# Optimization experiments

Measured on AMD Instinct MI355X. Metric: run time of the kernel, lower is better.

Reference implementation:

```python
import jax, jax.numpy as jnp
import numpy as np

NUM_EMBEDDINGS = 4096
EMBEDDING_DIM = 64
COMMITMENT_COST = 0.25
DECAY = 0.99
EPSILON = 1e-05


def setup_inputs() -> dict:
    key = jax.random.key(0)
    k1, k2, k3, k4 = jax.random.split(key, 4)
    z = jax.random.normal(k1, (128, 24, 1536), dtype=jnp.float32)
    embedding = jax.random.normal(k2, (NUM_EMBEDDINGS, EMBEDDING_DIM), dtype=jnp.float32) * 0.05
    ema_cluster_size = jax.random.uniform(k3, (NUM_EMBEDDINGS,), dtype=jnp.float32)
    ema_w = jax.random.normal(k4, (NUM_EMBEDDINGS, EMBEDDING_DIM), dtype=jnp.float32) * 0.05
    return {"z": z, "embedding": embedding, "ema_cluster_size": ema_cluster_size, "ema_w": ema_w}


def reference(z, embedding, ema_cluster_size, ema_w):
    # VectorQuantizer.forward in training mode (EMA codebook update).
    K, d = embedding.shape
    B = z.shape[0]
    z_flat = z.reshape(-1, d)  # [N, d], N = B*576

    # Pairwise squared distances: ||z||^2 + ||e||^2 - 2 z e^T  -> [N, K]
    dist = (jnp.sum(z_flat * z_flat, axis=1, keepdims=True)
            + jnp.sum(embedding * embedding, axis=1)
            - 2.0 * (z_flat @ embedding.T))
    codes = jnp.argmin(dist, axis=1)  # [N]

    # EMA statistics (one-hot scatter expressed as segment sums)
    counts = jax.ops.segment_sum(jnp.ones_like(codes, dtype=z.dtype), codes, num_segments=K)
    new_cluster_size = DECAY * ema_cluster_size + (1.0 - DECAY) * counts
    dw = jax.ops.segment_sum(z_flat, codes, num_segments=K)  # [K, d]
    new_ema_w = DECAY * ema_w + (1.0 - DECAY) * dw

    n = jnp.sum(new_cluster_size)
    cluster_size = (new_cluster_size + EPSILON) / (n + K * EPSILON) * n
    new_embedding = new_ema_w / cluster_size[:, None]

    # Quantize with the UPDATED codebook (torch copies weights before embedding lookup)
    z_q = new_embedding[codes].reshape(z.shape)
    vq_loss = COMMITMENT_COST * jnp.mean((jax.lax.stop_gradient(z_q) - z) ** 2)
    z_q_st = z + jax.lax.stop_gradient(z_q - z)  # straight-through
    codes = codes.reshape(B, -1)  # [B, 576]
    return (vq_loss, z_q_st, codes, new_embedding, new_cluster_size, new_ema_w)
```

## Files before the change

### kernel.cpp

```cpp
#include <hip/hip_runtime.h>

constexpr int KC    = 4096;
constexpr int DIM   = 64;
constexpr int NROWS = 73728;
constexpr int NELEM = 4718592;
constexpr int GSTRIDE = 4160;

typedef _Float16 f16x8 __attribute__((ext_vector_type(8)));
typedef float    f32x4 __attribute__((ext_vector_type(4)));

constexpr size_t OUT_LOSS  = 0;
constexpr size_t OUT_ZQ    = 1;
constexpr size_t OUT_CODES = 1 + (size_t)NELEM;
constexpr size_t OUT_EMB   = OUT_CODES + (size_t)NROWS;
constexpr size_t OUT_NCS   = OUT_EMB + (size_t)KC * DIM;
constexpr size_t OUT_NEW   = OUT_NCS + (size_t)KC;

constexpr size_t alignup(size_t x, size_t a) { return (x + a - 1) & ~(a - 1); }
constexpr size_t WS_CODES  = 0;
constexpr size_t WS_COUNTS = WS_CODES + sizeof(int) * (size_t)NROWS;
constexpr size_t WS_OFFS   = WS_COUNTS + sizeof(int) * (size_t)KC;
constexpr size_t WS_CURSOR = alignup(WS_OFFS + sizeof(int) * (KC + 1), 16);
constexpr size_t WS_SORTED = WS_CURSOR + sizeof(int) * (size_t)KC;
constexpr size_t WS_N      = alignup(WS_SORTED + sizeof(int) * (size_t)NROWS, 16);
constexpr size_t WS_LOSSD  = alignup(WS_N + sizeof(float), 8);
constexpr size_t WS_EMBPK  = alignup(WS_LOSSD + 8, 64);

__global__ void k_prep(const float* __restrict__ emb, char* __restrict__ emb_pk,
                       int* __restrict__ counts) {
    if (threadIdx.x < 32) counts[blockIdx.x * 32 + threadIdx.x] = 0;
    int t = blockIdx.x * 256 + threadIdx.x;
    int c = t >> 3, q = t & 7;
    const float* ep = emb + (size_t)c * DIM + q * 8;
    f16x8 hv, lv;
    float s = 0.f;
    #pragma unroll
    for (int e = 0; e < 8; ++e) {
        float x = ep[e];
        _Float16 h = (_Float16)x;
        float r = x - (float)h;
        hv[e] = h;
        lv[e] = (_Float16)(r * 2048.0f);
        s = fmaf(x, x, s);
    }
    s += __shfl_xor(s, 1, 64);
    s += __shfl_xor(s, 2, 64);
    s += __shfl_xor(s, 4, 64);
    int g = c >> 4, lc = c & 15;
    int h = q >> 2, lq = q & 3;
    int lane = lq * 16 + lc;
    char* gbase = emb_pk + (size_t)g * GSTRIDE;
    if (q == 0) *(float*)(gbase + lc * 4) = 1024.0f * s;
    char* base = gbase + 64 + lane * 16;
    *(f16x8*)(base + h * 1024)       = hv;
    *(f16x8*)(base + (2 + h) * 1024) = lv;
}

__global__ __launch_bounds__(192, 2) void k_argmin7(
        const float* __restrict__ z, const char* __restrict__ emb_pk,
        int* __restrict__ codes_i, float* __restrict__ codes_f,
        int* __restrict__ counts) {
    __shared__ int codebuf[3][48];

    const int tid = threadIdx.x;
    const int l   = tid & 63;
    const int w   = tid >> 6;
    const int lc  = l & 15;
    const int lq  = l >> 4;
    const int waveRow = blockIdx.x * 144 + w * 48;

    f16x8 ah2k[3][2], ahr[3][2], al2k[3][2];
    #pragma unroll
    for (int rt = 0; rt < 3; ++rt)
        #pragma unroll
        for (int h = 0; h < 2; ++h) {
            const float* zp = z + (size_t)(waveRow + rt * 16 + lc) * DIM + h * 32 + lq * 8;
            float4 x0 = *(const float4*)zp;
            float4 x1 = *(const float4*)(zp + 4);
            float xs[8] = {x0.x, x0.y, x0.z, x0.w, x1.x, x1.y, x1.z, x1.w};
            #pragma unroll
            for (int e = 0; e < 8; ++e) {
                _Float16 hh = (_Float16)xs[e];
                float rr = xs[e] - (float)hh;
                ahr[rt][h][e]  = -hh;
                ah2k[rt][h][e] = (_Float16)(-2048.0f * (float)hh);
                al2k[rt][h][e] = -(_Float16)(rr * 2048.0f);
            }
        }

    float best[3][4];
    int   bestg[3][4];
    #pragma unroll
    for (int rt = 0; rt < 3; ++rt)
        #pragma unroll
        for (int j = 0; j < 4; ++j) { best[rt][j] = INFINITY; bestg[rt][j] = 0; }

    const unsigned long long pkb = (unsigned long long)emb_pk;
    unsigned voffA = 64 + l * 16;
    unsigned voffB = lc * 4;

    f16x8 b00, b01, b02, b03, b10, b11, b12, b13;
    f16x8 b20, b21, b22, b23, b30, b31, b32, b33;
    float e0, e1, e2v, e3;

#define ISSUE(B0, B1, B2, B3, EV)                                                        \
    asm volatile("global_load_dword %0, %1, %2"             : "=v"(EV) : "v"(voffB), "s"(pkb)); \
    asm volatile("global_load_dwordx4 %0, %1, %2"             : "=v"(B0) : "v"(voffA), "s"(pkb)); \
    asm volatile("global_load_dwordx4 %0, %1, %2 offset:1024" : "=v"(B1) : "v"(voffA), "s"(pkb)); \
    asm volatile("global_load_dwordx4 %0, %1, %2 offset:2048" : "=v"(B2) : "v"(voffA), "s"(pkb)); \
    asm volatile("global_load_dwordx4 %0, %1, %2 offset:3072" : "=v"(B3) : "v"(voffA), "s"(pkb)); \
    voffA += GSTRIDE; voffB += GSTRIDE;

#define WAITP                                                \
    asm volatile("s_waitcnt vmcnt(15)" ::: "memory");        \
    __builtin_amdgcn_sched_barrier(0);

#define COMP(B0, B1, B2, B3, EV, G) {                                             \
        f32x4 ci; ci[0] = EV; ci[1] = EV; ci[2] = EV; ci[3] = EV;                 \
        _Pragma("unroll")                                                         \
        for (int rt = 0; rt < 3; ++rt) {                                          \
            f32x4 acc = __builtin_amdgcn_mfma_f32_16x16x32_f16(ah2k[rt][0], B0, ci, 0, 0, 0); \
            acc = __builtin_amdgcn_mfma_f32_16x16x32_f16(ah2k[rt][1], B1, acc, 0, 0, 0);      \
            acc = __builtin_amdgcn_mfma_f32_16x16x32_f16(ahr[rt][0],  B2, acc, 0, 0, 0);      \
            acc = __builtin_amdgcn_mfma_f32_16x16x32_f16(ahr[rt][1],  B3, acc, 0, 0, 0);      \
            acc = __builtin_amdgcn_mfma_f32_16x16x32_f16(al2k[rt][0], B0, acc, 0, 0, 0);      \
            acc = __builtin_amdgcn_mfma_f32_16x16x32_f16(al2k[rt][1], B1, acc, 0, 0, 0);      \
            _Pragma("unroll")                                                     \
            for (int j = 0; j < 4; ++j) {                                         \
                if (acc[j] < best[rt][j]) { best[rt][j] = acc[j]; bestg[rt][j] = (G); } \
            }                                                                     \
        } }

    __builtin_amdgcn_sched_barrier(0);
    ISSUE(b00, b01, b02, b03, e0)
    ISSUE(b10, b11, b12, b13, e1)
    ISSUE(b20, b21, b22, b23, e2v)
    ISSUE(b30, b31, b32, b33, e3)

    for (int g = 0; g < 256; g += 4) {
        WAITP  COMP(b00, b01, b02, b03, e0,  g)      ISSUE(b00, b01, b02, b03, e0)
        WAITP  COMP(b10, b11, b12, b13, e1,  g + 1)  ISSUE(b10, b11, b12, b13, e1)
        WAITP  COMP(b20, b21, b22, b23, e2v, g + 2)  ISSUE(b20, b21, b22, b23, e2v)
        WAITP  COMP(b30, b31, b32, b33, e3,  g + 3)  ISSUE(b30, b31, b32, b33, e3)
    }
    asm volatile("s_waitcnt vmcnt(0)" ::: "memory");
    __builtin_amdgcn_sched_barrier(0);
#undef ISSUE
#undef WAITP
#undef COMP

    #pragma unroll
    for (int rt = 0; rt < 3; ++rt)
        #pragma unroll
        for (int j = 0; j < 4; ++j) {
            float b = best[rt][j];
            int   k = bestg[rt][j] * 16 + lc;
            #pragma unroll
            for (int m = 1; m < 16; m <<= 1) {
                float obv = __shfl_xor(b, m, 64);
                int   okv = __shfl_xor(k, m, 64);
                if (obv < b || (obv == b && okv < k)) { b = obv; k = okv; }
            }
            if (lc == 0) codebuf[w][rt * 16 + lq * 4 + j] = k;
        }

    if (l < 48) {
        int code = codebuf[w][l];
        size_t rowg = (size_t)waveRow + l;
        codes_i[rowg] = code;
        codes_f[rowg] = (float)code;
        atomicAdd(&counts[code], 1);
    }
}

__global__ void k_scan(const int* __restrict__ counts,
                       int* __restrict__ offsets, int* __restrict__ cursor,
                       const float* __restrict__ ema_cs, float* __restrict__ ncs_out,
                       float* __restrict__ n_out, double* __restrict__ lossp) {
    __shared__ int   part[256];
    __shared__ float fpart[256];
    int tid = threadIdx.x;
    if (tid == 0) *lossp = 0.0;
    int base = tid * 16;
    int loc[16];
    int s = 0;
    float fs = 0.f;
    #pragma unroll
    for (int j = 0; j < 16; ++j) {
        int cnt = counts[base + j];
        loc[j] = s; s += cnt;
        float v = 0.99f * ema_cs[base + j] + 0.01f * (float)cnt;
        ncs_out[base + j] = v;
        fs += v;
    }
    part[tid] = s;
    fpart[tid] = fs;
    __syncthreads();
    for (int off = 1; off < 256; off <<= 1) {
        int v = (tid >= off) ? part[tid - off] : 0;
        __syncthreads();
        part[tid] += v;
        __syncthreads();
    }
    int excl = part[tid] - s;
    #pragma unroll
    for (int j = 0; j < 16; ++j) {
        int o = excl + loc[j];
        offsets[base + j] = o;
        cursor[base + j]  = o;
    }
    if (tid == 255) offsets[KC] = excl + s;
    for (int m = 128; m > 0; m >>= 1) {
        if (tid < m) fpart[tid] += fpart[tid + m];
        __syncthreads();
    }
    if (tid == 0) n_out[0] = fpart[0];
}

__global__ void k_scatteridx(const int* __restrict__ codes_i,
                             int* __restrict__ cursor, int* __restrict__ sorted_rows) {
    int r = blockIdx.x * 256 + threadIdx.x;
    if (r < NROWS) {
        int c = codes_i[r];
        int p = atomicAdd(&cursor[c], 1);
        sorted_rows[p] = r;
    }
}

__global__ __launch_bounds__(64) void k_dwsum(
        const float* __restrict__ z, const int* __restrict__ offsets,
        const int* __restrict__ sorted_rows, const float* __restrict__ ema_w,
        const float* __restrict__ ncs, const float* __restrict__ nptr,
        float* __restrict__ new_ema_w_out, float* __restrict__ new_emb_out) {
    int k = blockIdx.x, tid = threadIdx.x;
    int beg = offsets[k], end = offsets[k + 1];
    float a0 = 0.f, a1 = 0.f, a2 = 0.f, a3 = 0.f;
    int i = beg;
    for (; i + 3 < end; i += 4) {
        int r0 = sorted_rows[i], r1 = sorted_rows[i + 1];
        int r2 = sorted_rows[i + 2], r3 = sorted_rows[i + 3];
        a0 += z[(size_t)r0 * DIM + tid];
        a1 += z[(size_t)r1 * DIM + tid];
        a2 += z[(size_t)r2 * DIM + tid];
        a3 += z[(size_t)r3 * DIM + tid];
    }
    for (; i < end; ++i) a0 += z[(size_t)sorted_rows[i] * DIM + tid];
    float dwv = (a0 + a1) + (a2 + a3);
    size_t idx = (size_t)k * DIM + tid;
    float n = nptr[0];
    float nw = 0.99f * ema_w[idx] + 0.01f * dwv;
    float cs = (ncs[k] + 1e-5f) / (n + 4096.0f * 1e-5f) * n;
    new_ema_w_out[idx] = nw;
    new_emb_out[idx] = nw / cs;
}

__global__ __launch_bounds__(256) void k_quant(
        const float* __restrict__ z, const float* __restrict__ new_emb,
        const int* __restrict__ codes, float* __restrict__ zq_out,
        double* __restrict__ loss_acc) {
    __shared__ double red[256];
    const int nvec = NELEM / 4;
    int t = blockIdx.x * 256 + threadIdx.x;
    int stride = gridDim.x * 256;
    double ls = 0.0;
    for (int v = t; v < nvec; v += stride) {
        int e0 = v * 4;
        int n  = e0 >> 6;
        int d0 = e0 & 63;
        int code = codes[n];
        float4 zq = *(const float4*)&new_emb[(size_t)code * DIM + d0];
        float4 zv = *(const float4*)&z[e0];
        float dx = zq.x - zv.x, dy = zq.y - zv.y, dz = zq.z - zv.z, dw4 = zq.w - zv.w;
        float4 o;
        o.x = zv.x + dx; o.y = zv.y + dy; o.z = zv.z + dz; o.w = zv.w + dw4;
        *(float4*)&zq_out[e0] = o;
        ls += (double)(dx * dx) + (double)(dy * dy) + (double)(dz * dz) + (double)(dw4 * dw4);
    }
    red[threadIdx.x] = ls;
    __syncthreads();
    for (int m = 128; m > 0; m >>= 1) {
        if (threadIdx.x < m) red[threadIdx.x] += red[threadIdx.x + m];
        __syncthreads();
    }
    if (threadIdx.x == 0) atomicAdd(loss_acc, red[0]);
}

__global__ void k_loss(const double* __restrict__ loss_acc, float* __restrict__ out0) {
    out0[0] = (float)(0.25 * (loss_acc[0] / (double)NELEM));
}

extern "C" void kernel_launch(void* const* d_in, const int* in_sizes, int n_in,
                              void* d_out, int out_size, void* d_ws, size_t ws_size,
                              hipStream_t stream) {
    const float* z      = (const float*)d_in[0];
    const float* emb    = (const float*)d_in[1];
    const float* ema_cs = (const float*)d_in[2];
    const float* ema_w  = (const float*)d_in[3];
    float* out = (float*)d_out;
    char*  ws  = (char*)d_ws;

    int*    codes_i = (int*)(ws + WS_CODES);
    int*    counts  = (int*)(ws + WS_COUNTS);
    int*    offsets = (int*)(ws + WS_OFFS);
    int*    cursor  = (int*)(ws + WS_CURSOR);
    int*    sorted  = (int*)(ws + WS_SORTED);
    float*  nptr    = (float*)(ws + WS_N);
    double* lossp   = (double*)(ws + WS_LOSSD);
    char*   emb_pk  = ws + WS_EMBPK;

    k_prep<<<(KC * 8) / 256, 256, 0, stream>>>(emb, emb_pk, counts);
    k_argmin7<<<NROWS / 144, 192, 0, stream>>>(z, emb_pk, codes_i,
                                               out + OUT_CODES, counts);
    k_scan<<<1, 256, 0, stream>>>(counts, offsets, cursor, ema_cs,
                                  out + OUT_NCS, nptr, lossp);
    k_scatteridx<<<(NROWS + 255) / 256, 256, 0, stream>>>(codes_i, cursor, sorted);
    k_dwsum<<<KC, 64, 0, stream>>>(z, offsets, sorted, ema_w,
                                   out + OUT_NCS, nptr, out + OUT_NEW, out + OUT_EMB);
    k_quant<<<1152, 256, 0, stream>>>(z, out + OUT_EMB, codes_i,
                                      out + OUT_ZQ, lossp);
    k_loss<<<1, 1, 0, stream>>>(lossp, out + OUT_LOSS);
}
```

Measured before the change: 167.6 us.

## Stage codebook tiles into an LDS ring via direct global-to-LDS loads

The argmin kernel stops having every wave load the packed f16 codebook straight into registers. The three waves of a block now share a 12-slot LDS ring filled with global_load_lds DMA, and each wave reads operands back from LDS. The codebook norms move into a separate array that is preloaded whole into LDS. This removes the redundant per-wave global traffic for the codebook but adds a block barrier every four groups, LDS read latency, and roughly 64KB of LDS per block, which may limit occupancy to two blocks per CU.

```diff
diff --git a/kernel.cpp b/kernel.cpp
--- a/kernel.cpp
+++ b/kernel.cpp
@@ -4,7 +4,8 @@
 constexpr int DIM   = 64;
 constexpr int NROWS = 73728;
 constexpr int NELEM = 4718592;
-constexpr int GSTRIDE = 4160;
+constexpr int RB    = 4096;
+constexpr int RING  = 12;
 
 typedef _Float16 f16x8 __attribute__((ext_vector_type(8)));
 typedef float    f32x4 __attribute__((ext_vector_type(4)));
@@ -22,12 +23,19 @@
 constexpr size_t WS_OFFS   = WS_COUNTS + sizeof(int) * (size_t)KC;
 constexpr size_t WS_CURSOR = alignup(WS_OFFS + sizeof(int) * (KC + 1), 16);
 constexpr size_t WS_SORTED = WS_CURSOR + sizeof(int) * (size_t)KC;
-constexpr size_t WS_N      = alignup(WS_SORTED + sizeof(int) * (size_t)NROWS, 16);
+constexpr size_t WS_E2     = alignup(WS_SORTED + sizeof(int) * (size_t)NROWS, 64);
+constexpr size_t WS_N      = WS_E2 + sizeof(float) * (size_t)KC;
 constexpr size_t WS_LOSSD  = alignup(WS_N + sizeof(float), 8);
 constexpr size_t WS_EMBPK  = alignup(WS_LOSSD + 8, 64);
 
+__device__ __forceinline__ void gload16(const void* g, void* l) {
+    __builtin_amdgcn_global_load_lds(
+        (const __attribute__((address_space(1))) unsigned int*)g,
+        (__attribute__((address_space(3))) unsigned int*)l, 16, 0, 0);
+}
+
 __global__ void k_prep(const float* __restrict__ emb, char* __restrict__ emb_pk,
-                       int* __restrict__ counts) {
+                       float* __restrict__ e2s, int* __restrict__ counts) {
     if (threadIdx.x < 32) counts[blockIdx.x * 32 + threadIdx.x] = 0;
     int t = blockIdx.x * 256 + threadIdx.x;
     int c = t >> 3, q = t & 7;
@@ -46,21 +54,23 @@
     s += __shfl_xor(s, 1, 64);
     s += __shfl_xor(s, 2, 64);
     s += __shfl_xor(s, 4, 64);
+    if (q == 0) e2s[c] = 1024.0f * s;
     int g = c >> 4, lc = c & 15;
     int h = q >> 2, lq = q & 3;
     int lane = lq * 16 + lc;
-    char* gbase = emb_pk + (size_t)g * GSTRIDE;
-    if (q == 0) *(float*)(gbase + lc * 4) = 1024.0f * s;
-    char* base = gbase + 64 + lane * 16;
+    char* base = emb_pk + (size_t)g * RB + lane * 16;
     *(f16x8*)(base + h * 1024)       = hv;
     *(f16x8*)(base + (2 + h) * 1024) = lv;
 }
 
-__global__ __launch_bounds__(192, 2) void k_argmin7(
+__global__ __launch_bounds__(192, 2) void k_argmin8(
         const float* __restrict__ z, const char* __restrict__ emb_pk,
+        const float* __restrict__ e2s,
         int* __restrict__ codes_i, float* __restrict__ codes_f,
         int* __restrict__ counts) {
+    __shared__ __align__(16) char lds[RING * RB + 16384];
     __shared__ int codebuf[3][48];
+    constexpr int E2OFF = RING * RB;
 
     const int tid = threadIdx.x;
     const int l   = tid & 63;
@@ -95,25 +105,21 @@
         #pragma unroll
         for (int j = 0; j < 4; ++j) { best[rt][j] = INFINITY; bestg[rt][j] = 0; }
 
-    const unsigned long long pkb = (unsigned long long)emb_pk;
-    unsigned voffA = 64 + l * 16;
-    unsigned voffB = lc * 4;
-
-    f16x8 b00, b01, b02, b03, b10, b11, b12, b13;
-    f16x8 b20, b21, b22, b23, b30, b31, b32, b33;
-    float e0, e1, e2v, e3;
-
-#define ISSUE(B0, B1, B2, B3, EV)                                                        \
-    asm volatile("global_load_dword %0, %1, %2"             : "=v"(EV) : "v"(voffB), "s"(pkb)); \
-    asm volatile("global_load_dwordx4 %0, %1, %2"             : "=v"(B0) : "v"(voffA), "s"(pkb)); \
-    asm volatile("global_load_dwordx4 %0, %1, %2 offset:1024" : "=v"(B1) : "v"(voffA), "s"(pkb)); \
-    asm volatile("global_load_dwordx4 %0, %1, %2 offset:2048" : "=v"(B2) : "v"(voffA), "s"(pkb)); \
-    asm volatile("global_load_dwordx4 %0, %1, %2 offset:3072" : "=v"(B3) : "v"(voffA), "s"(pkb)); \
-    voffA += GSTRIDE; voffB += GSTRIDE;
-
-#define WAITP                                                \
-    asm volatile("s_waitcnt vmcnt(15)" ::: "memory");        \
-    __builtin_amdgcn_sched_barrier(0);
+#define STAGE(GS) {                                                         \
+        int slot_ = (GS) % RING;                                            \
+        int gsrc_ = (GS) < 256 ? (GS) : 255;                                \
+        const char* gp_ = emb_pk + (size_t)gsrc_ * RB + (l << 4);           \
+        char* lp_ = lds + slot_ * RB;                                       \
+        gload16(gp_ + w * 1024, lp_ + w * 1024);                            \
+        gload16(gp_ + 3072,     lp_ + 3072); }
+
+#define LOADL(EV, B0, B1, B2, B3, G) {                                      \
+        const char* p_ = lds + ((G) % RING) * RB + (l << 4);                \
+        B0 = *(const f16x8*)(p_);                                           \
+        B1 = *(const f16x8*)(p_ + 1024);                                    \
+        B2 = *(const f16x8*)(p_ + 2048);                                    \
+        B3 = *(const f16x8*)(p_ + 3072);                                    \
+        EV = *(const float*)(lds + E2OFF + (((G) * 16 + lc) << 2)); }
 
 #define COMP(B0, B1, B2, B3, EV, G) {                                             \
         f32x4 ci; ci[0] = EV; ci[1] = EV; ci[2] = EV; ci[3] = EV;                 \
@@ -131,22 +137,35 @@
             }                                                                     \
         } }
 
+    for (int s = w; s < 16; s += 3)
+        gload16((const char*)e2s + s * 1024 + (l << 4), lds + E2OFF + s * 1024);
+    for (int gs = 0; gs < 8; ++gs) STAGE(gs);
+    asm volatile("s_waitcnt vmcnt(16)" ::: "memory");
+    __builtin_amdgcn_s_barrier();
     __builtin_amdgcn_sched_barrier(0);
-    ISSUE(b00, b01, b02, b03, e0)
-    ISSUE(b10, b11, b12, b13, e1)
-    ISSUE(b20, b21, b22, b23, e2v)
-    ISSUE(b30, b31, b32, b33, e3)
-
-    for (int g = 0; g < 256; g += 4) {
-        WAITP  COMP(b00, b01, b02, b03, e0,  g)      ISSUE(b00, b01, b02, b03, e0)
-        WAITP  COMP(b10, b11, b12, b13, e1,  g + 1)  ISSUE(b10, b11, b12, b13, e1)
-        WAITP  COMP(b20, b21, b22, b23, e2v, g + 2)  ISSUE(b20, b21, b22, b23, e2v)
-        WAITP  COMP(b30, b31, b32, b33, e3,  g + 3)  ISSUE(b30, b31, b32, b33, e3)
+
+    {
+        f16x8 A0, A1, A2, A3, B0, B1, B2, B3;
+        float eA, eB;
+        for (int t = 0; t < 256; t += 4) {
+            asm volatile("s_waitcnt vmcnt(8)" ::: "memory");
+            __builtin_amdgcn_s_barrier();
+            __builtin_amdgcn_sched_barrier(0);
+            LOADL(eA, A0, A1, A2, A3, t);
+            LOADL(eB, B0, B1, B2, B3, t + 1);
+            COMP(A0, A1, A2, A3, eA, t);
+            LOADL(eA, A0, A1, A2, A3, t + 2);
+            COMP(B0, B1, B2, B3, eB, t + 1);
+            LOADL(eB, B0, B1, B2, B3, t + 3);
+            COMP(A0, A1, A2, A3, eA, t + 2);
+            COMP(B0, B1, B2, B3, eB, t + 3);
+            STAGE(t + 8) STAGE(t + 9) STAGE(t + 10) STAGE(t + 11)
+        }
     }
     asm volatile("s_waitcnt vmcnt(0)" ::: "memory");
     __builtin_amdgcn_sched_barrier(0);
-#undef ISSUE
-#undef WAITP
+#undef STAGE
+#undef LOADL
 #undef COMP
 
     #pragma unroll
@@ -304,12 +323,13 @@
     int*    offsets = (int*)(ws + WS_OFFS);
     int*    cursor  = (int*)(ws + WS_CURSOR);
     int*    sorted  = (int*)(ws + WS_SORTED);
+    float*  e2s     = (float*)(ws + WS_E2);
     float*  nptr    = (float*)(ws + WS_N);
     double* lossp   = (double*)(ws + WS_LOSSD);
     char*   emb_pk  = ws + WS_EMBPK;
 
-    k_prep<<<(KC * 8) / 256, 256, 0, stream>>>(emb, emb_pk, counts);
-    k_argmin7<<<NROWS / 144, 192, 0, stream>>>(z, emb_pk, codes_i,
+    k_prep<<<(KC * 8) / 256, 256, 0, stream>>>(emb, emb_pk, e2s, counts);
+    k_argmin8<<<NROWS / 144, 192, 0, stream>>>(z, emb_pk, e2s, codes_i,
                                                out + OUT_CODES, counts);
     k_scan<<<1, 256, 0, stream>>>(counts, offsets, cursor, ema_cs,
                                   out + OUT_NCS, nptr, lossp);
```

New measurement: 177.8 us. 1.06x slower.

## Split codebook search across two waves per row tile and merge via LDS

Applied to the files above, without the earlier changes.

The argmin kernel changes from three waves each scanning the full codebook for their own 48 rows to two waves sharing the same 48 rows, each scanning half the codebook. A shared-memory merge then picks the better candidate per row. This doubles the block count and halves the serial loop length per wave, raising parallelism and shortening tail latency. The cost is re-converting the same z rows in both waves, an extra __syncthreads and merge, and wasted prefetches that wrap back to the start of each half.

```diff
diff --git a/kernel.cpp b/kernel.cpp
--- a/kernel.cpp
+++ b/kernel.cpp
@@ -56,18 +56,20 @@
     *(f16x8*)(base + (2 + h) * 1024) = lv;
 }
 
-__global__ __launch_bounds__(192, 2) void k_argmin7(
+__global__ __launch_bounds__(128, 2) void k_argmin11(
         const float* __restrict__ z, const char* __restrict__ emb_pk,
         int* __restrict__ codes_i, float* __restrict__ codes_f,
         int* __restrict__ counts) {
-    __shared__ int codebuf[3][48];
+    __shared__ float bd[2][48];
+    __shared__ int   bk[2][48];
 
     const int tid = threadIdx.x;
     const int l   = tid & 63;
     const int w   = tid >> 6;
     const int lc  = l & 15;
     const int lq  = l >> 4;
-    const int waveRow = blockIdx.x * 144 + w * 48;
+    const int waveRow = blockIdx.x * 48;
+    const int gBase   = w * 128;
 
     f16x8 ah2k[3][2], ahr[3][2], al2k[3][2];
     #pragma unroll
@@ -96,8 +98,10 @@
         for (int j = 0; j < 4; ++j) { best[rt][j] = INFINITY; bestg[rt][j] = 0; }
 
     const unsigned long long pkb = (unsigned long long)emb_pk;
-    unsigned voffA = 64 + l * 16;
-    unsigned voffB = lc * 4;
+    const unsigned voffA0 = (unsigned)(gBase * GSTRIDE) + 64 + l * 16;
+    const unsigned voffB0 = (unsigned)(gBase * GSTRIDE) + lc * 4;
+    unsigned voffA = voffA0;
+    unsigned voffB = voffB0;
 
     f16x8 b00, b01, b02, b03, b10, b11, b12, b13;
     f16x8 b20, b21, b22, b23, b30, b31, b32, b33;
@@ -137,11 +141,13 @@
     ISSUE(b20, b21, b22, b23, e2v)
     ISSUE(b30, b31, b32, b33, e3)
 
-    for (int g = 0; g < 256; g += 4) {
-        WAITP  COMP(b00, b01, b02, b03, e0,  g)      ISSUE(b00, b01, b02, b03, e0)
-        WAITP  COMP(b10, b11, b12, b13, e1,  g + 1)  ISSUE(b10, b11, b12, b13, e1)
-        WAITP  COMP(b20, b21, b22, b23, e2v, g + 2)  ISSUE(b20, b21, b22, b23, e2v)
-        WAITP  COMP(b30, b31, b32, b33, e3,  g + 3)  ISSUE(b30, b31, b32, b33, e3)
+    #pragma unroll 1
+    for (int g = 0; g < 128; g += 4) {
+        if (g == 124) { voffA = voffA0; voffB = voffB0; }
+        WAITP  COMP(b00, b01, b02, b03, e0,  gBase + g)      ISSUE(b00, b01, b02, b03, e0)
+        WAITP  COMP(b10, b11, b12, b13, e1,  gBase + g + 1)  ISSUE(b10, b11, b12, b13, e1)
+        WAITP  COMP(b20, b21, b22, b23, e2v, gBase + g + 2)  ISSUE(b20, b21, b22, b23, e2v)
+        WAITP  COMP(b30, b31, b32, b33, e3,  gBase + g + 3)  ISSUE(b30, b31, b32, b33, e3)
     }
     asm volatile("s_waitcnt vmcnt(0)" ::: "memory");
     __builtin_amdgcn_sched_barrier(0);
@@ -161,12 +167,18 @@
                 int   okv = __shfl_xor(k, m, 64);
                 if (obv < b || (obv == b && okv < k)) { b = obv; k = okv; }
             }
-            if (lc == 0) codebuf[w][rt * 16 + lq * 4 + j] = k;
+            if (lc == 0) {
+                bd[w][rt * 16 + lq * 4 + j] = b;
+                bk[w][rt * 16 + lq * 4 + j] = k;
+            }
         }
-
-    if (l < 48) {
-        int code = codebuf[w][l];
-        size_t rowg = (size_t)waveRow + l;
+    __syncthreads();
+
+    if (tid < 48) {
+        float d0 = bd[0][tid], d1 = bd[1][tid];
+        int   k0 = bk[0][tid], k1 = bk[1][tid];
+        int code = (d1 < d0) ? k1 : k0;
+        size_t rowg = (size_t)waveRow + tid;
         codes_i[rowg] = code;
         codes_f[rowg] = (float)code;
         atomicAdd(&counts[code], 1);
@@ -309,7 +321,7 @@
     char*   emb_pk  = ws + WS_EMBPK;
 
     k_prep<<<(KC * 8) / 256, 256, 0, stream>>>(emb, emb_pk, counts);
-    k_argmin7<<<NROWS / 144, 192, 0, stream>>>(z, emb_pk, codes_i,
+    k_argmin11<<<NROWS / 48, 128, 0, stream>>>(z, emb_pk, codes_i,
                                                out + OUT_CODES, counts);
     k_scan<<<1, 256, 0, stream>>>(counts, offsets, cursor, ema_cs,
                                   out + OUT_NCS, nptr, lossp);
```

Result: slower. 180.3 us (+7.6%).

## Switch argmin distance GEMM to 32x32x16 MFMA with repacked codebook layout

Applied to the files above, without the earlier changes.

Replaces the 16x16x32 MFMA tiling (3 row tiles of 16 per wave, 16 codes per group) with 32x32x16 MFMA tiles (32 rows by 32 codes per wave). The packed codebook layout moves to 8 KB groups, and the ||e||^2 values go into a separate array. The loop becomes a two-stage double buffer with a wraparound prefetch. The aim is fewer MFMA and compare instructions per code and better operand reuse. In exchange each wave covers fewer rows (32 instead of 48) and each block has fewer waves, and the argmin reduction now needs a 32-lane shuffle.

```diff
diff --git a/kernel.cpp b/kernel.cpp
--- a/kernel.cpp
+++ b/kernel.cpp
@@ -4,10 +4,10 @@
 constexpr int DIM   = 64;
 constexpr int NROWS = 73728;
 constexpr int NELEM = 4718592;
-constexpr int GSTRIDE = 4160;
-
-typedef _Float16 f16x8 __attribute__((ext_vector_type(8)));
-typedef float    f32x4 __attribute__((ext_vector_type(4)));
+constexpr int GB    = 8192;
+
+typedef _Float16 f16x8  __attribute__((ext_vector_type(8)));
+typedef float    f32x16 __attribute__((ext_vector_type(16)));
 
 constexpr size_t OUT_LOSS  = 0;
 constexpr size_t OUT_ZQ    = 1;
@@ -22,12 +22,13 @@
 constexpr size_t WS_OFFS   = WS_COUNTS + sizeof(int) * (size_t)KC;
 constexpr size_t WS_CURSOR = alignup(WS_OFFS + sizeof(int) * (KC + 1), 16);
 constexpr size_t WS_SORTED = WS_CURSOR + sizeof(int) * (size_t)KC;
-constexpr size_t WS_N      = alignup(WS_SORTED + sizeof(int) * (size_t)NROWS, 16);
+constexpr size_t WS_E2     = alignup(WS_SORTED + sizeof(int) * (size_t)NROWS, 64);
+constexpr size_t WS_N      = WS_E2 + sizeof(float) * (size_t)KC;
 constexpr size_t WS_LOSSD  = alignup(WS_N + sizeof(float), 8);
 constexpr size_t WS_EMBPK  = alignup(WS_LOSSD + 8, 64);
 
 __global__ void k_prep(const float* __restrict__ emb, char* __restrict__ emb_pk,
-                       int* __restrict__ counts) {
+                       float* __restrict__ e2s, int* __restrict__ counts) {
     if (threadIdx.x < 32) counts[blockIdx.x * 32 + threadIdx.x] = 0;
     int t = blockIdx.x * 256 + threadIdx.x;
     int c = t >> 3, q = t & 7;
@@ -46,125 +47,134 @@
     s += __shfl_xor(s, 1, 64);
     s += __shfl_xor(s, 2, 64);
     s += __shfl_xor(s, 4, 64);
-    int g = c >> 4, lc = c & 15;
-    int h = q >> 2, lq = q & 3;
-    int lane = lq * 16 + lc;
-    char* gbase = emb_pk + (size_t)g * GSTRIDE;
-    if (q == 0) *(float*)(gbase + lc * 4) = 1024.0f * s;
-    char* base = gbase + 64 + lane * 16;
-    *(f16x8*)(base + h * 1024)       = hv;
-    *(f16x8*)(base + (2 + h) * 1024) = lv;
-}
-
-__global__ __launch_bounds__(192, 2) void k_argmin7(
+    if (q == 0) e2s[c] = 1024.0f * s;
+    int g2 = c >> 5, col = c & 31;
+    int cc = q >> 1, h2 = q & 1;
+    int lane = h2 * 32 + col;
+    char* base = emb_pk + (size_t)g2 * GB + cc * 1024 + lane * 16;
+    *(f16x8*)base            = hv;
+    *(f16x8*)(base + 4096)   = lv;
+}
+
+__global__ __launch_bounds__(128, 2) void k_argmin13(
         const float* __restrict__ z, const char* __restrict__ emb_pk,
+        const float* __restrict__ e2s,
         int* __restrict__ codes_i, float* __restrict__ codes_f,
         int* __restrict__ counts) {
-    __shared__ int codebuf[3][48];
+    __shared__ int codebuf[2][32];
 
     const int tid = threadIdx.x;
     const int l   = tid & 63;
     const int w   = tid >> 6;
-    const int lc  = l & 15;
-    const int lq  = l >> 4;
-    const int waveRow = blockIdx.x * 144 + w * 48;
-
-    f16x8 ah2k[3][2], ahr[3][2], al2k[3][2];
-    #pragma unroll
-    for (int rt = 0; rt < 3; ++rt)
+    const int col = l & 31;
+    const int h2  = l >> 5;
+    const int waveRow = blockIdx.x * 64 + w * 32;
+
+    f16x8 ah2k[4], ahr[4], al2k[4];
+    #pragma unroll
+    for (int c = 0; c < 4; ++c) {
+        const float* zp = z + (size_t)(waveRow + col) * DIM + c * 16 + h2 * 8;
+        float4 x0 = *(const float4*)zp;
+        float4 x1 = *(const float4*)(zp + 4);
+        float xs[8] = {x0.x, x0.y, x0.z, x0.w, x1.x, x1.y, x1.z, x1.w};
         #pragma unroll
-        for (int h = 0; h < 2; ++h) {
-            const float* zp = z + (size_t)(waveRow + rt * 16 + lc) * DIM + h * 32 + lq * 8;
-            float4 x0 = *(const float4*)zp;
-            float4 x1 = *(const float4*)(zp + 4);
-            float xs[8] = {x0.x, x0.y, x0.z, x0.w, x1.x, x1.y, x1.z, x1.w};
-            #pragma unroll
-            for (int e = 0; e < 8; ++e) {
-                _Float16 hh = (_Float16)xs[e];
-                float rr = xs[e] - (float)hh;
-                ahr[rt][h][e]  = -hh;
-                ah2k[rt][h][e] = (_Float16)(-2048.0f * (float)hh);
-                al2k[rt][h][e] = -(_Float16)(rr * 2048.0f);
-            }
+        for (int e = 0; e < 8; ++e) {
+            _Float16 hh = (_Float16)xs[e];
+            float rr = xs[e] - (float)hh;
+            ahr[c][e]  = -hh;
+            ah2k[c][e] = (_Float16)(-2048.0f * (float)hh);
+            al2k[c][e] = -(_Float16)(rr * 2048.0f);
         }
-
-    float best[3][4];
-    int   bestg[3][4];
-    #pragma unroll
-    for (int rt = 0; rt < 3; ++rt)
-        #pragma unroll
-        for (int j = 0; j < 4; ++j) { best[rt][j] = INFINITY; bestg[rt][j] = 0; }
+    }
+
+    float best[16];
+    int   bestg[16];
+    #pragma unroll
+    for (int r = 0; r < 16; ++r) { best[r] = INFINITY; bestg[r] = 0; }
 
     const unsigned long long pkb = (unsigned long long)emb_pk;
-    unsigned voffA = 64 + l * 16;
-    unsigned voffB = lc * 4;
-
-    f16x8 b00, b01, b02, b03, b10, b11, b12, b13;
-    f16x8 b20, b21, b22, b23, b30, b31, b32, b33;
-    float e0, e1, e2v, e3;
-
-#define ISSUE(B0, B1, B2, B3, EV)                                                        \
-    asm volatile("global_load_dword %0, %1, %2"             : "=v"(EV) : "v"(voffB), "s"(pkb)); \
+    const unsigned long long e2b = (unsigned long long)e2s;
+    unsigned voffA = l * 16;
+    unsigned voffA2 = 4096 + l * 16;
+    unsigned voffB = col * 4;
+
+    f16x8 a0, a1, a2, a3, a4, a5, a6, a7;
+    f16x8 c0, c1, c2, c3, c4, c5, c6, c7;
+    float eA, eB;
+
+#define ISSUE(B0, B1, B2, B3, B4, B5, B6, B7, EV)                                          \
+    asm volatile("global_load_dword %0, %1, %2"               : "=v"(EV) : "v"(voffB), "s"(e2b)); \
     asm volatile("global_load_dwordx4 %0, %1, %2"             : "=v"(B0) : "v"(voffA), "s"(pkb)); \
     asm volatile("global_load_dwordx4 %0, %1, %2 offset:1024" : "=v"(B1) : "v"(voffA), "s"(pkb)); \
     asm volatile("global_load_dwordx4 %0, %1, %2 offset:2048" : "=v"(B2) : "v"(voffA), "s"(pkb)); \
     asm volatile("global_load_dwordx4 %0, %1, %2 offset:3072" : "=v"(B3) : "v"(voffA), "s"(pkb)); \
-    voffA += GSTRIDE; voffB += GSTRIDE;
+    asm volatile("global_load_dwordx4 %0, %1, %2"             : "=v"(B4) : "v"(voffA2), "s"(pkb)); \
+    asm volatile("global_load_dwordx4 %0, %1, %2 offset:1024" : "=v"(B5) : "v"(voffA2), "s"(pkb)); \
+    asm volatile("global_load_dwordx4 %0, %1, %2 offset:2048" : "=v"(B6) : "v"(voffA2), "s"(pkb)); \
+    asm volatile("global_load_dwordx4 %0, %1, %2 offset:3072" : "=v"(B7) : "v"(voffA2), "s"(pkb)); \
+    voffA += GB; voffA2 += GB; voffB += 128;
+
+#define WRAP0 { voffA = l * 16; voffA2 = 4096 + l * 16; voffB = col * 4; }
 
 #define WAITP                                                \
-    asm volatile("s_waitcnt vmcnt(15)" ::: "memory");        \
+    asm volatile("s_waitcnt vmcnt(9)" ::: "memory");         \
     __builtin_amdgcn_sched_barrier(0);
 
-#define COMP(B0, B1, B2, B3, EV, G) {                                             \
-        f32x4 ci; ci[0] = EV; ci[1] = EV; ci[2] = EV; ci[3] = EV;                 \
-        _Pragma("unroll")                                                         \
-        for (int rt = 0; rt < 3; ++rt) {                                          \
-            f32x4 acc = __builtin_amdgcn_mfma_f32_16x16x32_f16(ah2k[rt][0], B0, ci, 0, 0, 0); \
-            acc = __builtin_amdgcn_mfma_f32_16x16x32_f16(ah2k[rt][1], B1, acc, 0, 0, 0);      \
-            acc = __builtin_amdgcn_mfma_f32_16x16x32_f16(ahr[rt][0],  B2, acc, 0, 0, 0);      \
-            acc = __builtin_amdgcn_mfma_f32_16x16x32_f16(ahr[rt][1],  B3, acc, 0, 0, 0);      \
-            acc = __builtin_amdgcn_mfma_f32_16x16x32_f16(al2k[rt][0], B0, acc, 0, 0, 0);      \
-            acc = __builtin_amdgcn_mfma_f32_16x16x32_f16(al2k[rt][1], B1, acc, 0, 0, 0);      \
-            _Pragma("unroll")                                                     \
-            for (int j = 0; j < 4; ++j) {                                         \
-                if (acc[j] < best[rt][j]) { best[rt][j] = acc[j]; bestg[rt][j] = (G); } \
-            }                                                                     \
-        } }
+#define COMP(B0, B1, B2, B3, B4, B5, B6, B7, EV, G) {                                      \
+        f32x16 acc;                                                                        \
+        _Pragma("unroll")                                                                  \
+        for (int r = 0; r < 16; ++r) acc[r] = EV;                                          \
+        acc = __builtin_amdgcn_mfma_f32_32x32x16_f16(ah2k[0], B0, acc, 0, 0, 0);           \
+        acc = __builtin_amdgcn_mfma_f32_32x32x16_f16(ah2k[1], B1, acc, 0, 0, 0);           \
+        acc = __builtin_amdgcn_mfma_f32_32x32x16_f16(ah2k[2], B2, acc, 0, 0, 0);           \
+        acc = __builtin_amdgcn_mfma_f32_32x32x16_f16(ah2k[3], B3, acc, 0, 0, 0);           \
+        acc = __builtin_amdgcn_mfma_f32_32x32x16_f16(ahr[0],  B4, acc, 0, 0, 0);           \
+        acc = __builtin_amdgcn_mfma_f32_32x32x16_f16(ahr[1],  B5, acc, 0, 0, 0);           \
+        acc = __builtin_amdgcn_mfma_f32_32x32x16_f16(ahr[2],  B6, acc, 0, 0, 0);           \
+        acc = __builtin_amdgcn_mfma_f32_32x32x16_f16(ahr[3],  B7, acc, 0, 0, 0);           \
+        acc = __builtin_amdgcn_mfma_f32_32x32x16_f16(al2k[0], B0, acc, 0, 0, 0);           \
+        acc = __builtin_amdgcn_mfma_f32_32x32x16_f16(al2k[1], B1, acc, 0, 0, 0);           \
+        acc = __builtin_amdgcn_mfma_f32_32x32x16_f16(al2k[2], B2, acc, 0, 0, 0);           \
+        acc = __builtin_amdgcn_mfma_f32_32x32x16_f16(al2k[3], B3, acc, 0, 0, 0);           \
+        _Pragma("unroll")                                                                  \
+        for (int r = 0; r < 16; ++r)                                                       \
+            if (acc[r] < best[r]) { best[r] = acc[r]; bestg[r] = (G); }                    \
+    }
 
     __builtin_amdgcn_sched_barrier(0);
-    ISSUE(b00, b01, b02, b03, e0)
-    ISSUE(b10, b11, b12, b13, e1)
-    ISSUE(b20, b21, b22, b23, e2v)
-    ISSUE(b30, b31, b32, b33, e3)
-
-    for (int g = 0; g < 256; g += 4) {
-        WAITP  COMP(b00, b01, b02, b03, e0,  g)      ISSUE(b00, b01, b02, b03, e0)
-        WAITP  COMP(b10, b11, b12, b13, e1,  g + 1)  ISSUE(b10, b11, b12, b13, e1)
-        WAITP  COMP(b20, b21, b22, b23, e2v, g + 2)  ISSUE(b20, b21, b22, b23, e2v)
-        WAITP  COMP(b30, b31, b32, b33, e3,  g + 3)  ISSUE(b30, b31, b32, b33, e3)
+    ISSUE(a0, a1, a2, a3, a4, a5, a6, a7, eA)
+
+    #pragma unroll 1
+    for (int g = 0; g < 128; g += 2) {
+        ISSUE(c0, c1, c2, c3, c4, c5, c6, c7, eB)
+        WAITP
+        COMP(a0, a1, a2, a3, a4, a5, a6, a7, eA, g)
+        if (g == 126) WRAP0
+        ISSUE(a0, a1, a2, a3, a4, a5, a6, a7, eA)
+        WAITP
+        COMP(c0, c1, c2, c3, c4, c5, c6, c7, eB, g + 1)
     }
     asm volatile("s_waitcnt vmcnt(0)" ::: "memory");
     __builtin_amdgcn_sched_barrier(0);
 #undef ISSUE
+#undef WRAP0
 #undef WAITP
 #undef COMP
 
     #pragma unroll
-    for (int rt = 0; rt < 3; ++rt)
+    for (int r = 0; r < 16; ++r) {
+        float b = best[r];
+        int   k = bestg[r] * 32 + col;
         #pragma unroll
-        for (int j = 0; j < 4; ++j) {
-            float b = best[rt][j];
-            int   k = bestg[rt][j] * 16 + lc;
-            #pragma unroll
-            for (int m = 1; m < 16; m <<= 1) {
-                float obv = __shfl_xor(b, m, 64);
-                int   okv = __shfl_xor(k, m, 64);
-                if (obv < b || (obv == b && okv < k)) { b = obv; k = okv; }
-            }
-            if (lc == 0) codebuf[w][rt * 16 + lq * 4 + j] = k;
+        for (int m = 1; m < 32; m <<= 1) {
+            float obv = __shfl_xor(b, m, 64);
+            int   okv = __shfl_xor(k, m, 64);
+            if (obv < b || (obv == b && okv < k)) { b = obv; k = okv; }
         }
-
-    if (l < 48) {
+        if (col == 0) codebuf[w][(r & 3) + 8 * (r >> 2) + 4 * h2] = k;
+    }
+
+    if (l < 32) {
         int code = codebuf[w][l];
         size_t rowg = (size_t)waveRow + l;
         codes_i[rowg] = code;
@@ -304,12 +314,13 @@
     int*    offsets = (int*)(ws + WS_OFFS);
     int*    cursor  = (int*)(ws + WS_CURSOR);
     int*    sorted  = (int*)(ws + WS_SORTED);
+    float*  e2s     = (float*)(ws + WS_E2);
     float*  nptr    = (float*)(ws + WS_N);
     double* lossp   = (double*)(ws + WS_LOSSD);
     char*   emb_pk  = ws + WS_EMBPK;
 
-    k_prep<<<(KC * 8) / 256, 256, 0, stream>>>(emb, emb_pk, counts);
-    k_argmin7<<<NROWS / 144, 192, 0, stream>>>(z, emb_pk, codes_i,
+    k_prep<<<(KC * 8) / 256, 256, 0, stream>>>(emb, emb_pk, e2s, counts);
+    k_argmin13<<<NROWS / 64, 128, 0, stream>>>(z, emb_pk, e2s, codes_i,
                                                out + OUT_CODES, counts);
     k_scan<<<1, 256, 0, stream>>>(counts, offsets, cursor, ema_cs,
                                   out + OUT_NCS, nptr, lossp);
```

Measured after the change: 214.7 us. +28.1%, slower.
